# Kernel tuning notes

Hardware: AMD Instinct MI355X
Metric: run time of the kernel (lower is better)

Reference implementation:

```python
import jax, jax.numpy as jnp
import numpy as np

KEEP_RATIO = 0.8  # layer_threshold output at representative progress
NEG = -10000.0


def _extract(h, a, m):
    # h: [B,S,H] float, a: [B,S] float additive mask, m: [B,S] bool keep-mask
    # Torch version compacts to max_len = m.sum(-1).max(); here we pad the
    # compacted width to the static S (extra slots masked), same math.
    B, S, H = h.shape
    mi = m.astype(jnp.int32)
    c = jnp.cumsum(mi, axis=-1) * mi               # [B,S] dest slot (+1), 0 = dropped
    brow = jnp.arange(B)[:, None]
    amin = a.min()
    new_a = jnp.full((B, S + 1), amin, a.dtype).at[brow, c].set(a)[:, 1:]
    ar = jnp.broadcast_to(jnp.arange(S, dtype=jnp.int32), (B, S))
    index = jnp.full((B, S + 1), S, jnp.int32).at[brow, c].set(ar)[:, 1:]
    new_h = jnp.zeros((B, S + 1, H), h.dtype).at[brow, c].set(h)[:, 1:]
    return new_h, new_a, index


def _unextract(large, small, index):
    # scatter compacted `small` rows back into a copy of `large` at `index`;
    # index == S points at a sacrificial padded row that is dropped.
    B, S = large.shape[0], large.shape[1]
    brow = jnp.arange(B)[:, None]
    if large.ndim == 3:
        pad = jnp.zeros((B, 1, large.shape[2]), large.dtype)
    else:
        pad = jnp.zeros((B, 1), large.dtype)
    dest = jnp.concatenate([large, pad], axis=1)
    dest = dest.at[brow, index].set(small)
    return dest[:, :-1]


def _topk_mask(scores, attention_mask, keep_ratio):
    # keep top ceil-ish (tokens*ratio, >=1) scoring tokens per row
    B, S = scores.shape
    s = scores + attention_mask
    tokens = (attention_mask == 0).sum(1).astype(jnp.float32) * keep_ratio
    tokens = jnp.maximum(tokens.astype(jnp.int32), 1)            # [B]
    keep_first = jnp.arange(S, dtype=jnp.int32)[None, :] < tokens[:, None]
    order = jnp.argsort(-s, axis=1).astype(jnp.int32)            # descending sort indices
    idx = (order + 1) * keep_first.astype(jnp.int32)             # dropped -> slot 0
    brow = jnp.arange(B)[:, None]
    final = jnp.zeros((B, S + 1), jnp.float32).at[brow, idx].set(1.0)
    return final[:, 1:]


def setup_inputs() -> dict:
    key = jax.random.key(0)
    k1, k2, k3, k4 = jax.random.split(key, 4)
    B, S, H = 8, 4096, 1024
    hidden_states = jax.random.normal(k1, (B, S, H), dtype=jnp.float32)
    lengths = jax.random.randint(k2, (B,), S // 2, S + 1)
    valid = jnp.arange(S)[None, :] < lengths[:, None]
    attention_mask = jnp.where(valid, 0.0, NEG).astype(jnp.float32)
    keep = jax.random.uniform(k3, (B, S)) < 0.8
    previous_mask = (valid & keep).astype(jnp.float32).at[:, 0].set(1.0)
    W = (jax.random.normal(k4, (H, H), dtype=jnp.float32) / np.float32(np.sqrt(H)))
    b = jnp.zeros((H,), dtype=jnp.float32)
    return {"hidden_states": hidden_states, "attention_mask": attention_mask,
            "previous_mask": previous_mask, "W": W, "b": b}


def reference(hidden_states, attention_mask, previous_mask, W, b):
    m = previous_mask > 0.5
    sub_h, sub_a, sub_index = _extract(hidden_states, attention_mask, m)
    ret0 = sub_h  # child transformer layer abstracted to identity
    scores = jnp.max(jnp.einsum('bsh,hk->bsk', sub_h, W) + b, axis=-1) + sub_a * 100.0
    mask = _topk_mask(scores, sub_a, KEEP_RATIO)
    new_mask = _unextract(previous_mask, mask, sub_index)
    new_ret = _unextract(hidden_states, ret0, sub_index)
    return new_ret, new_mask
```

## Files before the change

### kernel.cpp

```cpp
#include <hip/hip_runtime.h>
#include <stdint.h>

static constexpr int BB = 8;
static constexpr int SS = 4096;
static constexpr int HH = 1024;

__device__ __forceinline__ unsigned f2mono(float f) {
    unsigned u = __float_as_uint(f);
    return (u & 0x80000000u) ? ~u : (u | 0x80000000u);
}
__device__ __forceinline__ float mono2f(unsigned u) {
    return __uint_as_float((u & 0x80000000u) ? (u ^ 0x80000000u) : ~u);
}

__global__ void reduce_ab(const float* __restrict__ a, const float* __restrict__ bias,
                          float* __restrict__ amin_out, float* __restrict__ bmax_out) {
    __shared__ float red[256];
    int t = threadIdx.x;
    float mn = 1e30f;
    for (int i = t; i < BB * SS; i += 256) mn = fminf(mn, a[i]);
    red[t] = mn; __syncthreads();
    for (int o = 128; o; o >>= 1) { if (t < o) red[t] = fminf(red[t], red[t + o]); __syncthreads(); }
    if (t == 0) *amin_out = red[0];
    __syncthreads();
    float mx = -1e30f;
    for (int i = t; i < HH; i += 256) mx = fmaxf(mx, bias[i]);
    red[t] = mx; __syncthreads();
    for (int o = 128; o; o >>= 1) { if (t < o) red[t] = fmaxf(red[t], red[t + o]); __syncthreads(); }
    if (t == 0) *bmax_out = red[0];
}

__global__ void compact(const float* __restrict__ prev, const float* __restrict__ a,
                        int* __restrict__ kept_src, unsigned* __restrict__ scores,
                        int* __restrict__ n_keep, int* __restrict__ zcnt) {
    int b = blockIdx.x;
    int lane = threadIdx.x;
    const float* pm = prev + (size_t)b * SS;
    const float* am = a + (size_t)b * SS;
    int* ks = kept_src + (size_t)b * SS;

    int base_s = lane * (SS / 64);
    int cnt = 0, zc = 0;
    for (int i = 0; i < SS / 64; ++i) {
        if (pm[base_s + i] > 0.5f) {
            cnt++;
            if (am[base_s + i] == 0.0f) zc++;
        }
    }
    int incl = cnt;
    for (int o = 1; o < 64; o <<= 1) {
        int v = __shfl_up(incl, o);
        if (lane >= o) incl += v;
    }
    int total = __shfl(incl, 63);
    int pos = incl - cnt;
    for (int i = 0; i < SS / 64; ++i) {
        if (pm[base_s + i] > 0.5f) ks[pos++] = base_s + i;
    }
    for (int o = 1; o < 64; o <<= 1) zc += __shfl_xor(zc, o);
    if (lane == 0) { n_keep[b] = total; zcnt[b] = zc; }
    for (int j = total + lane; j < SS; j += 64) ks[j] = 0;
    unsigned* sc = scores + (size_t)b * SS;
    for (int j = lane; j < SS; j += 64) sc[j] = 0u;
}

#define MT 32
#define NT 256
__global__ __launch_bounds__(256) void gemm_max(
    const float* __restrict__ hs, const float* __restrict__ W,
    const float* __restrict__ bias, const int* __restrict__ kept_src,
    const int* __restrict__ n_keep, unsigned* __restrict__ scores) {
    int mt = blockIdx.x;
    int nt = blockIdx.y;
    int b  = blockIdx.z;
    int nk = n_keep[b];
    int m0 = mt * MT;
    if (m0 >= nk) return;

    __shared__ float A[32][MT];
    __shared__ int src[MT];
    int t  = threadIdx.x;
    int tn = t & 63;
    int tm = t >> 6;
    if (t < MT) src[t] = kept_src[(size_t)b * SS + m0 + t];
    __syncthreads();

    float acc[32];
#pragma unroll
    for (int i = 0; i < 32; ++i) acc[i] = 0.f;

    int n0 = nt * NT;
    const float* wp = W + n0 + tn * 4;
    int sm = t >> 3;
    int kq = t & 7;
    const float* myrow = hs + ((size_t)b * SS + (size_t)src[sm]) * HH + kq * 4;

    for (int kc = 0; kc < HH / 32; ++kc) {
        float4 f = *(const float4*)(myrow + kc * 32);
        A[kq * 4 + 0][sm] = f.x; A[kq * 4 + 1][sm] = f.y;
        A[kq * 4 + 2][sm] = f.z; A[kq * 4 + 3][sm] = f.w;
        __syncthreads();
        const float* wk = wp + (size_t)kc * 32 * HH;
#pragma unroll 4
        for (int k = 0; k < 32; ++k) {
            float4 w4 = *(const float4*)wk;
            wk += HH;
            const float4* ar = (const float4*)(&A[k][tm * 8]);
            float4 a0 = ar[0], a1 = ar[1];
            float av[8] = {a0.x, a0.y, a0.z, a0.w, a1.x, a1.y, a1.z, a1.w};
            float wv[4] = {w4.x, w4.y, w4.z, w4.w};
#pragma unroll
            for (int i = 0; i < 8; ++i)
#pragma unroll
                for (int c = 0; c < 4; ++c)
                    acc[i * 4 + c] = fmaf(av[i], wv[c], acc[i * 4 + c]);
        }
        __syncthreads();
    }

    float4 bia = *(const float4*)(bias + n0 + tn * 4);
    float bv[4] = {bia.x, bia.y, bia.z, bia.w};
#pragma unroll
    for (int i = 0; i < 8; ++i) {
        float v = -1e30f;
#pragma unroll
        for (int c = 0; c < 4; ++c) v = fmaxf(v, acc[i * 4 + c] + bv[c]);
        for (int o = 32; o; o >>= 1) v = fmaxf(v, __shfl_xor(v, o));
        if (tn == 0)
            atomicMax(scores + (size_t)b * SS + m0 + tm * 8 + i, f2mono(v));
    }
}

__global__ __launch_bounds__(1024) void topk_scatter(
    const float* __restrict__ a, const float* __restrict__ prev,
    const int* __restrict__ kept_src, const unsigned* __restrict__ scores,
    const int* __restrict__ n_keep, const int* __restrict__ zcnt,
    const float* __restrict__ amin_p, const float* __restrict__ bmax_p,
    float* __restrict__ out_mask) {
    __shared__ unsigned long long keys[SS];
    int b = blockIdx.x;
    int t = threadIdx.x;
    int nk = n_keep[b];
    float amin = *amin_p, bmax = *bmax_p;
    int z = zcnt[b] + ((amin == 0.0f) ? (SS - nk) : 0);
    int tk = (int)((float)z * 0.8f);
    if (tk < 1) tk = 1;
    float padv = (bmax + amin * 100.0f) + amin;

    const int* ks = kept_src + (size_t)b * SS;
    const unsigned* sc = scores + (size_t)b * SS;
    const float* arow = a + (size_t)b * SS;

    for (int j = t; j < SS; j += 1024) {
        float sval;
        if (j < nk) {
            float core = mono2f(sc[j]);
            float av = arow[ks[j]];
            sval = (core + av * 100.0f) + av;
        } else {
            sval = padv;
        }
        keys[j] = ((unsigned long long)(~f2mono(sval)) << 32) | (unsigned)j;
    }
    float* om = out_mask + (size_t)b * SS;
    const float* pm = prev + (size_t)b * SS;
    for (int j = t; j < SS; j += 1024) om[j] = pm[j];
    __syncthreads();

    for (int k = 2; k <= SS; k <<= 1) {
        for (int jj = k >> 1; jj > 0; jj >>= 1) {
            for (int i = t; i < SS; i += 1024) {
                int ixj = i ^ jj;
                if (ixj > i) {
                    bool up = ((i & k) == 0);
                    unsigned long long x = keys[i], y = keys[ixj];
                    if ((x > y) == up) { keys[i] = y; keys[ixj] = x; }
                }
            }
            __syncthreads();
        }
    }

    for (int p = t; p < SS; p += 1024) {
        int j = (int)(keys[p] & 0xFFFFFFFFull);
        if (j < nk) om[ks[j]] = (p < tk) ? 1.0f : 0.0f;
    }
}

extern "C" void kernel_launch(void* const* d_in, const int* in_sizes, int n_in,
                              void* d_out, int out_size, void* d_ws, size_t ws_size,
                              hipStream_t stream) {
    const float* hs   = (const float*)d_in[0];
    const float* am   = (const float*)d_in[1];
    const float* pmsk = (const float*)d_in[2];
    const float* W    = (const float*)d_in[3];
    const float* bias = (const float*)d_in[4];

    float* out0 = (float*)d_out;
    float* out1 = out0 + (size_t)BB * SS * HH;

    char* ws = (char*)d_ws;
    int*      kept_src = (int*)ws;
    unsigned* scores   = (unsigned*)(ws + (size_t)BB * SS * 4);
    int*      nkeep    = (int*)(ws + (size_t)2 * BB * SS * 4);
    int*      zc       = nkeep + BB;
    float*    amin_p   = (float*)(zc + BB);
    float*    bmax_p   = amin_p + 1;

    hipMemcpyAsync(out0, hs, (size_t)BB * SS * HH * sizeof(float),
                   hipMemcpyDeviceToDevice, stream);

    hipLaunchKernelGGL(reduce_ab, dim3(1), dim3(256), 0, stream, am, bias, amin_p, bmax_p);
    hipLaunchKernelGGL(compact, dim3(BB), dim3(64), 0, stream,
                       pmsk, am, kept_src, scores, nkeep, zc);
    hipLaunchKernelGGL(gemm_max, dim3(SS / MT, HH / NT, BB), dim3(256), 0, stream,
                       hs, W, bias, kept_src, nkeep, scores);
    hipLaunchKernelGGL(topk_scatter, dim3(BB), dim3(1024), 0, stream,
                       am, pmsk, kept_src, scores, nkeep, zc, amin_p, bmax_p, out1);
}
```

Before: 947.4 us.

## Replace bitonic top-k with parallel rank counting and enlarge GEMM tile

Replaces the single-block-per-batch bitonic sort with a rank-counting top-k. Each of four blocks per batch computes every key's rank by scanning all keys in shared memory, which spreads the selection over more workgroups. The GEMM tile grows to 64 rows with 16 accumulator rows per wave to raise reuse of W loads, and the per-chunk syncs are rearranged. Score zeroing and the mask copy move into a separate grid-wide init kernel, and the amin reduction is vectorised. The rank scan does O(S^2) comparisons per batch, which is extra work, and the larger tile means more registers per thread and fewer blocks.

Measured after the change: 999.4 us. +5.5%, slower.

```diff
diff --git a/kernel.cpp b/kernel.cpp
--- a/kernel.cpp
+++ b/kernel.cpp
@@ -11,6 +11,12 @@
 }
 __device__ __forceinline__ float mono2f(unsigned u) {
     return __uint_as_float((u & 0x80000000u) ? (u ^ 0x80000000u) : ~u);
+}
+
+__global__ void k_init(const float* __restrict__ prev, unsigned* __restrict__ scores,
+                       float* __restrict__ out_mask) {
+    int i = blockIdx.x * blockDim.x + threadIdx.x;
+    if (i < BB * SS) { scores[i] = 0u; out_mask[i] = prev[i]; }
 }
 
 __global__ void reduce_ab(const float* __restrict__ a, const float* __restrict__ bias,
@@ -18,7 +24,11 @@
     __shared__ float red[256];
     int t = threadIdx.x;
     float mn = 1e30f;
-    for (int i = t; i < BB * SS; i += 256) mn = fminf(mn, a[i]);
+    const float4* a4 = (const float4*)a;
+    for (int i = t; i < BB * SS / 4; i += 256) {
+        float4 v = a4[i];
+        mn = fminf(mn, fminf(fminf(v.x, v.y), fminf(v.z, v.w)));
+    }
     red[t] = mn; __syncthreads();
     for (int o = 128; o; o >>= 1) { if (t < o) red[t] = fminf(red[t], red[t + o]); __syncthreads(); }
     if (t == 0) *amin_out = red[0];
@@ -31,7 +41,7 @@
 }
 
 __global__ void compact(const float* __restrict__ prev, const float* __restrict__ a,
-                        int* __restrict__ kept_src, unsigned* __restrict__ scores,
+                        int* __restrict__ kept_src,
                         int* __restrict__ n_keep, int* __restrict__ zcnt) {
     int b = blockIdx.x;
     int lane = threadIdx.x;
@@ -60,86 +70,88 @@
     for (int o = 1; o < 64; o <<= 1) zc += __shfl_xor(zc, o);
     if (lane == 0) { n_keep[b] = total; zcnt[b] = zc; }
     for (int j = total + lane; j < SS; j += 64) ks[j] = 0;
-    unsigned* sc = scores + (size_t)b * SS;
-    for (int j = lane; j < SS; j += 64) sc[j] = 0u;
-}
-
-#define MT 32
-#define NT 256
+}
+
+#define BM 64
+#define BN 256
+#define BK 32
+#define LDA 68
 __global__ __launch_bounds__(256) void gemm_max(
     const float* __restrict__ hs, const float* __restrict__ W,
     const float* __restrict__ bias, const int* __restrict__ kept_src,
     const int* __restrict__ n_keep, unsigned* __restrict__ scores) {
-    int mt = blockIdx.x;
-    int nt = blockIdx.y;
-    int b  = blockIdx.z;
+    int mt = blockIdx.x, nt = blockIdx.y, b = blockIdx.z;
     int nk = n_keep[b];
-    int m0 = mt * MT;
+    int m0 = mt * BM;
     if (m0 >= nk) return;
 
-    __shared__ float A[32][MT];
-    __shared__ int src[MT];
-    int t  = threadIdx.x;
-    int tn = t & 63;
-    int tm = t >> 6;
-    if (t < MT) src[t] = kept_src[(size_t)b * SS + m0 + t];
+    __shared__ float A[BK][LDA];
+    __shared__ int src[BM];
+    int t = threadIdx.x;
+    int lane = t & 63, w = t >> 6;
+    if (t < BM) src[t] = kept_src[(size_t)b * SS + m0 + t];
     __syncthreads();
 
-    float acc[32];
-#pragma unroll
-    for (int i = 0; i < 32; ++i) acc[i] = 0.f;
-
-    int n0 = nt * NT;
-    const float* wp = W + n0 + tn * 4;
-    int sm = t >> 3;
-    int kq = t & 7;
-    const float* myrow = hs + ((size_t)b * SS + (size_t)src[sm]) * HH + kq * 4;
-
-    for (int kc = 0; kc < HH / 32; ++kc) {
-        float4 f = *(const float4*)(myrow + kc * 32);
-        A[kq * 4 + 0][sm] = f.x; A[kq * 4 + 1][sm] = f.y;
-        A[kq * 4 + 2][sm] = f.z; A[kq * 4 + 3][sm] = f.w;
+    int srow = t >> 2;
+    int skq  = t & 3;
+    const float* arow = hs + ((size_t)b * SS + (size_t)src[srow]) * HH + skq * 8;
+    int n0 = nt * BN;
+    const float* wcol = W + n0 + lane * 4;
+
+    float acc[16][4];
+#pragma unroll
+    for (int r = 0; r < 16; ++r)
+#pragma unroll
+        for (int c = 0; c < 4; ++c) acc[r][c] = 0.f;
+
+    for (int kc = 0; kc < HH / BK; ++kc) {
+        float4 f0 = *(const float4*)(arow + kc * BK);
+        float4 f1 = *(const float4*)(arow + kc * BK + 4);
         __syncthreads();
-        const float* wk = wp + (size_t)kc * 32 * HH;
+        int kb = skq * 8;
+        A[kb + 0][srow] = f0.x; A[kb + 1][srow] = f0.y;
+        A[kb + 2][srow] = f0.z; A[kb + 3][srow] = f0.w;
+        A[kb + 4][srow] = f1.x; A[kb + 5][srow] = f1.y;
+        A[kb + 6][srow] = f1.z; A[kb + 7][srow] = f1.w;
+        __syncthreads();
+        const float* wk = wcol + (size_t)kc * BK * HH;
 #pragma unroll 4
-        for (int k = 0; k < 32; ++k) {
+        for (int k = 0; k < BK; ++k) {
             float4 w4 = *(const float4*)wk;
             wk += HH;
-            const float4* ar = (const float4*)(&A[k][tm * 8]);
-            float4 a0 = ar[0], a1 = ar[1];
-            float av[8] = {a0.x, a0.y, a0.z, a0.w, a1.x, a1.y, a1.z, a1.w};
+            const float4* ap = (const float4*)(&A[k][w * 16]);
+            float4 a0 = ap[0], a1 = ap[1], a2 = ap[2], a3 = ap[3];
+            float av[16] = {a0.x, a0.y, a0.z, a0.w, a1.x, a1.y, a1.z, a1.w,
+                            a2.x, a2.y, a2.z, a2.w, a3.x, a3.y, a3.z, a3.w};
             float wv[4] = {w4.x, w4.y, w4.z, w4.w};
 #pragma unroll
-            for (int i = 0; i < 8; ++i)
+            for (int r = 0; r < 16; ++r)
 #pragma unroll
                 for (int c = 0; c < 4; ++c)
-                    acc[i * 4 + c] = fmaf(av[i], wv[c], acc[i * 4 + c]);
+                    acc[r][c] = fmaf(av[r], wv[c], acc[r][c]);
         }
-        __syncthreads();
-    }
-
-    float4 bia = *(const float4*)(bias + n0 + tn * 4);
+    }
+
+    float4 bia = *(const float4*)(bias + n0 + lane * 4);
     float bv[4] = {bia.x, bia.y, bia.z, bia.w};
 #pragma unroll
-    for (int i = 0; i < 8; ++i) {
+    for (int r = 0; r < 16; ++r) {
         float v = -1e30f;
 #pragma unroll
-        for (int c = 0; c < 4; ++c) v = fmaxf(v, acc[i * 4 + c] + bv[c]);
+        for (int c = 0; c < 4; ++c) v = fmaxf(v, acc[r][c] + bv[c]);
         for (int o = 32; o; o >>= 1) v = fmaxf(v, __shfl_xor(v, o));
-        if (tn == 0)
-            atomicMax(scores + (size_t)b * SS + m0 + tm * 8 + i, f2mono(v));
-    }
-}
-
-__global__ __launch_bounds__(1024) void topk_scatter(
-    const float* __restrict__ a, const float* __restrict__ prev,
-    const int* __restrict__ kept_src, const unsigned* __restrict__ scores,
-    const int* __restrict__ n_keep, const int* __restrict__ zcnt,
-    const float* __restrict__ amin_p, const float* __restrict__ bmax_p,
-    float* __restrict__ out_mask) {
+        if (lane == 0)
+            atomicMax(scores + (size_t)b * SS + m0 + w * 16 + r, f2mono(v));
+    }
+}
+
+__global__ __launch_bounds__(1024) void topk_rank(
+    const float* __restrict__ a, const int* __restrict__ kept_src,
+    const unsigned* __restrict__ scores, const int* __restrict__ n_keep,
+    const int* __restrict__ zcnt, const float* __restrict__ amin_p,
+    const float* __restrict__ bmax_p, float* __restrict__ out_mask) {
     __shared__ unsigned long long keys[SS];
-    int b = blockIdx.x;
-    int t = threadIdx.x;
+    int b = blockIdx.x, ch = blockIdx.y, t = threadIdx.x;
     int nk = n_keep[b];
     float amin = *amin_p, bmax = *bmax_p;
     int z = zcnt[b] + ((amin == 0.0f) ? (SS - nk) : 0);
@@ -162,29 +174,15 @@
         }
         keys[j] = ((unsigned long long)(~f2mono(sval)) << 32) | (unsigned)j;
     }
-    float* om = out_mask + (size_t)b * SS;
-    const float* pm = prev + (size_t)b * SS;
-    for (int j = t; j < SS; j += 1024) om[j] = pm[j];
     __syncthreads();
 
-    for (int k = 2; k <= SS; k <<= 1) {
-        for (int jj = k >> 1; jj > 0; jj >>= 1) {
-            for (int i = t; i < SS; i += 1024) {
-                int ixj = i ^ jj;
-                if (ixj > i) {
-                    bool up = ((i & k) == 0);
-                    unsigned long long x = keys[i], y = keys[ixj];
-                    if ((x > y) == up) { keys[i] = y; keys[ixj] = x; }
-                }
-            }
-            __syncthreads();
-        }
-    }
-
-    for (int p = t; p < SS; p += 1024) {
-        int j = (int)(keys[p] & 0xFFFFFFFFull);
-        if (j < nk) om[ks[j]] = (p < tk) ? 1.0f : 0.0f;
-    }
+    int j = ch * 1024 + t;
+    unsigned long long mykey = keys[j];
+    int rank = 0;
+#pragma unroll 8
+    for (int i = 0; i < SS; ++i) rank += (keys[i] < mykey) ? 1 : 0;
+
+    if (j < nk) out_mask[(size_t)b * SS + ks[j]] = (rank < tk) ? 1.0f : 0.0f;
 }
 
 extern "C" void kernel_launch(void* const* d_in, const int* in_sizes, int n_in,
@@ -210,11 +208,13 @@
     hipMemcpyAsync(out0, hs, (size_t)BB * SS * HH * sizeof(float),
                    hipMemcpyDeviceToDevice, stream);
 
+    hipLaunchKernelGGL(k_init, dim3(BB * SS / 256), dim3(256), 0, stream,
+                       pmsk, scores, out1);
     hipLaunchKernelGGL(reduce_ab, dim3(1), dim3(256), 0, stream, am, bias, amin_p, bmax_p);
     hipLaunchKernelGGL(compact, dim3(BB), dim3(64), 0, stream,
-                       pmsk, am, kept_src, scores, nkeep, zc);
-    hipLaunchKernelGGL(gemm_max, dim3(SS / MT, HH / NT, BB), dim3(256), 0, stream,
+                       pmsk, am, kept_src, nkeep, zc);
+    hipLaunchKernelGGL(gemm_max, dim3(SS / BM, HH / BN, BB), dim3(256), 0, stream,
                        hs, W, bias, kept_src, nkeep, scores);
-    hipLaunchKernelGGL(topk_scatter, dim3(BB), dim3(1024), 0, stream,
-                       am, pmsk, kept_src, scores, nkeep, zc, amin_p, bmax_p, out1);
-}
+    hipLaunchKernelGGL(topk_rank, dim3(BB, SS / 1024), dim3(1024), 0, stream,
+                       am, kept_src, scores, nkeep, zc, amin_p, bmax_p, out1);
+}
```
